# Kernel optimization log

Measured on AMD Instinct MI355X. Metric: run time of the kernel, lower is better.

## Reference

```python
import jax, jax.numpy as jnp
import numpy as np

D_K = 64

def setup_inputs() -> dict:
    key = jax.random.key(0)
    kq, kk, kv = jax.random.split(key, 3)
    B, Lq, Lk, d = 32, 2048, 2048, D_K
    return {
        "query": jax.random.normal(kq, (B, Lq, d), dtype=jnp.float32),
        "key": jax.random.normal(kk, (B, Lk, d), dtype=jnp.float32),
        "value": jax.random.normal(kv, (B, Lk, d), dtype=jnp.float32),
    }

def reference(query, key, value):
    d_k = query.shape[-1]
    scale = 1.0 / jnp.sqrt(jnp.asarray(d_k, query.dtype))
    scores = jnp.einsum('nqd,nkd->nqk', query, key) * scale  # (B, Lq, Lk)
    attn = jax.nn.softmax(scores, axis=-1)  # masked=None -> plain softmax; dropout p=0.0 is identity
    return jnp.einsum('nqk,nkd->nqd', attn, value)  # (B, Lq, d_v)
```

## Files before the change

### kernel.cpp

```cpp
#include <hip/hip_runtime.h>


#define NB   32
#define LSEQ 2048
#define DH   64
#define BM   64
#define BN   64
#define NIT  (LSEQ / BN)

typedef __attribute__((ext_vector_type(8)))  __bf16 bf16x8;
typedef __attribute__((ext_vector_type(16))) float  f32x16;

union BF8 { bf16x8 v; unsigned short u[8]; unsigned u32[4]; uint4 q; };

__device__ __forceinline__ unsigned short f2bf(float f) {
    unsigned int u = __builtin_bit_cast(unsigned int, f);
    u += 0x7fffu + ((u >> 16) & 1u);
    return (unsigned short)(u >> 16);
}

__device__ __forceinline__ unsigned pack_bf2(float a, float b) {
    unsigned ua = __builtin_bit_cast(unsigned, a) + 0x8000u;
    unsigned ub = __builtin_bit_cast(unsigned, b) + 0x8000u;
    return __builtin_amdgcn_perm(ub, ua, 0x07060302u);
}

__device__ __forceinline__ float fast_exp2(float x) {
#if __has_builtin(__builtin_amdgcn_exp2f)
    return __builtin_amdgcn_exp2f(x);
#else
    return exp2f(x);
#endif
}

__device__ __forceinline__ void load_lds16(const void* g, void* l) {
    __builtin_amdgcn_global_load_lds(
        (const __attribute__((address_space(1))) void*)g,
        (__attribute__((address_space(3))) void*)l, 16, 0, 0);
}

#define KBLK ((NB * LSEQ * DH) / (256 * 8))
__global__ __launch_bounds__(256)
void prep(const float* __restrict__ Kg, const float* __restrict__ Vg,
          unsigned short* __restrict__ Kb, unsigned short* __restrict__ Vt) {
    __shared__ unsigned short T[64 * 65];
    const int tid = threadIdx.x;
    if (blockIdx.x < KBLK) {
        const size_t idx = ((size_t)blockIdx.x * 256 + tid) * 8;
        float4 f0 = ((const float4*)(Kg + idx))[0];
        float4 f1 = ((const float4*)(Kg + idx))[1];
        BF8 t;
        t.u[0]=f2bf(f0.x); t.u[1]=f2bf(f0.y); t.u[2]=f2bf(f0.z); t.u[3]=f2bf(f0.w);
        t.u[4]=f2bf(f1.x); t.u[5]=f2bf(f1.y); t.u[6]=f2bf(f1.z); t.u[7]=f2bf(f1.w);
        *(bf16x8*)&Kb[idx] = t.v;
    } else {
        const int bx = blockIdx.x - KBLK;
        const int b  = bx >> 5;
        const int nt = bx & 31;
        const int nl = tid >> 2;
        const int dc = (tid & 3) * 16;
        const float* src = Vg + (((size_t)b * LSEQ + nt * 64 + nl) * DH + dc);
        float4 f0 = ((const float4*)src)[0];
        float4 f1 = ((const float4*)src)[1];
        float4 f2 = ((const float4*)src)[2];
        float4 f3 = ((const float4*)src)[3];
        float vv[16] = {f0.x,f0.y,f0.z,f0.w, f1.x,f1.y,f1.z,f1.w,
                        f2.x,f2.y,f2.z,f2.w, f3.x,f3.y,f3.z,f3.w};
        #pragma unroll
        for (int i = 0; i < 16; ++i)
            T[(dc + i) * 65 + nl] = f2bf(vv[i]);
        __syncthreads();
        #pragma unroll
        for (int i = 0; i < 2; ++i) {
            const int CH = i * 256 + tid;
            const int d  = CH >> 3;
            const int cc = CH & 7;
            const int nloc = (cc ^ (d & 7)) * 8;
            BF8 o;
            #pragma unroll
            for (int j = 0; j < 8; ++j) o.u[j] = T[d * 65 + nloc + j];
            *(bf16x8*)&Vt[(((size_t)(b * 64 + d)) * 256 + nt * 8 + cc) * 8] = o.v;
        }
    }
}

__global__ __launch_bounds__(256, 4)
void attn_fwd(const unsigned short* __restrict__ Kb,
              const unsigned short* __restrict__ Vt,
              const float* __restrict__ Qg,
              float* __restrict__ Og) {
    __shared__ __align__(16) unsigned short Vlds[2][BN * DH];
    __shared__ __align__(16) float Mrg[2][64][36];
    __shared__ float Lsh[2][32];

    const int tid  = threadIdx.x;
    const int wave = tid >> 6;
    const int lane = tid & 63;
    const int m32  = lane & 31;
    const int h    = lane >> 5;
    const int qh   = wave >> 1;
    const int kvh  = wave & 1;
    const int b    = blockIdx.y;
    const int qt   = blockIdx.x;

    const float qscale = 0.18033688011112042f;
    const int qrow = qt * BM + qh * 32 + m32;
    bf16x8 qf[4];
    {
        const float* qp = Qg + ((size_t)(b * LSEQ + qrow)) * DH;
        #pragma unroll
        for (int kt = 0; kt < 4; ++kt) {
            const float* p4 = qp + kt * 16 + h * 8;
            float4 f0 = ((const float4*)p4)[0];
            float4 f1 = ((const float4*)p4)[1];
            BF8 t;
            t.u[0]=f2bf(f0.x*qscale); t.u[1]=f2bf(f0.y*qscale);
            t.u[2]=f2bf(f0.z*qscale); t.u[3]=f2bf(f0.w*qscale);
            t.u[4]=f2bf(f1.x*qscale); t.u[5]=f2bf(f1.y*qscale);
            t.u[6]=f2bf(f1.z*qscale); t.u[7]=f2bf(f1.w*qscale);
            qf[kt] = t.v;
        }
    }

    const char* kptr = (const char*)Kb
        + ((size_t)b * LSEQ + (kvh * 32 + m32)) * (DH * 2) + h * 16;

    int vidx[2][2];
    #pragma unroll
    for (int dt = 0; dt < 2; ++dt)
        #pragma unroll
        for (int kt = 0; kt < 2; ++kt) {
            const int d  = dt * 32 + m32;
            const int cc = kvh * 4 + kt * 2 + h;
            vidx[dt][kt] = (d * 8 + (cc ^ (d & 7))) * 8;
        }

    const char* vgb = (const char*)Vt + (size_t)b * (DH * LSEQ * 2);
    const int CH0 = wave * 128 + lane;
    const int CH1 = CH0 + 64;
    const int voff0 = (CH0 >> 3) * (LSEQ * 2) + (CH0 & 7) * 16;
    const int voff1 = (CH1 >> 3) * (LSEQ * 2) + (CH1 & 7) * 16;
    load_lds16(vgb + voff0, (char*)&Vlds[0][0] + wave * 2048);
    load_lds16(vgb + voff1, (char*)&Vlds[0][0] + wave * 2048 + 1024);

    f32x16 o0, o1;
    #pragma unroll
    for (int i = 0; i < 16; ++i) { o0[i] = 0.f; o1[i] = 0.f; }
    float l_run = 0.f;

    for (int nt = 0; nt < NIT; ++nt) {
        const int cur = nt & 1;
        __syncthreads();

        BF8 kf[4];
        {
            const char* ka = kptr + nt * (BN * DH * 2);
            #pragma unroll
            for (int kt = 0; kt < 4; ++kt)
                kf[kt].q = *(const uint4*)(ka + kt * 32);
        }
        if (nt + 1 < NIT) {
            char* vl = (char*)&Vlds[cur ^ 1][0] + wave * 2048;
            load_lds16(vgb + (nt + 1) * 128 + voff0, vl);
            load_lds16(vgb + (nt + 1) * 128 + voff1, vl + 1024);
        }

        f32x16 s;
        #pragma unroll
        for (int i = 0; i < 16; ++i) s[i] = 0.f;
        #pragma unroll
        for (int kt = 0; kt < 4; ++kt)
            s = __builtin_amdgcn_mfma_f32_32x32x16_bf16(kf[kt].v, qf[kt], s, 0, 0, 0);

        BF8 vf[2][2];
        #pragma unroll
        for (int dt = 0; dt < 2; ++dt)
            #pragma unroll
            for (int kt = 0; kt < 2; ++kt)
                vf[dt][kt].v = *(const bf16x8*)&Vlds[cur][vidx[dt][kt]];

        float e[16];
        #pragma unroll
        for (int r = 0; r < 16; ++r) e[r] = fast_exp2(s[r]);
        #pragma unroll
        for (int g = 0; g < 4; ++g)
            l_run += ((e[4*g] + e[4*g+1]) + (e[4*g+2] + e[4*g+3]));
        unsigned pk[8];
        #pragma unroll
        for (int g = 0; g < 4; ++g) {
            pk[2*g]   = pack_bf2(e[4*g],   e[4*g+1]);
            pk[2*g+1] = pack_bf2(e[4*g+2], e[4*g+3]);
        }

        const unsigned sA0 = h ? pk[0] : pk[2];
        const unsigned sA1 = h ? pk[1] : pk[3];
        const unsigned sB0 = h ? pk[4] : pk[6];
        const unsigned sB1 = h ? pk[5] : pk[7];
        const unsigned rA0 = __shfl_xor((int)sA0, 32, 64);
        const unsigned rA1 = __shfl_xor((int)sA1, 32, 64);
        const unsigned rB0 = __shfl_xor((int)sB0, 32, 64);
        const unsigned rB1 = __shfl_xor((int)sB1, 32, 64);
        BF8 p0, p1;
        p0.u32[0] = h ? rA0 : pk[0];  p0.u32[1] = h ? rA1 : pk[1];
        p0.u32[2] = h ? pk[2] : rA0;  p0.u32[3] = h ? pk[3] : rA1;
        p1.u32[0] = h ? rB0 : pk[4];  p1.u32[1] = h ? rB1 : pk[5];
        p1.u32[2] = h ? pk[6] : rB0;  p1.u32[3] = h ? pk[7] : rB1;

        o0 = __builtin_amdgcn_mfma_f32_32x32x16_bf16(vf[0][0].v, p0.v, o0, 0, 0, 0);
        o0 = __builtin_amdgcn_mfma_f32_32x32x16_bf16(vf[0][1].v, p1.v, o0, 0, 0, 0);
        o1 = __builtin_amdgcn_mfma_f32_32x32x16_bf16(vf[1][0].v, p0.v, o1, 0, 0, 0);
        o1 = __builtin_amdgcn_mfma_f32_32x32x16_bf16(vf[1][1].v, p1.v, o1, 0, 0, 0);
    }

    const float l2 = l_run + __shfl_xor(l_run, 32, 64);
    if (kvh) {
        float* mp = &Mrg[qh][lane][0];
        #pragma unroll
        for (int g = 0; g < 4; ++g) {
            *(float4*)(mp + 4*g)      = (float4){o0[4*g], o0[4*g+1], o0[4*g+2], o0[4*g+3]};
            *(float4*)(mp + 16 + 4*g) = (float4){o1[4*g], o1[4*g+1], o1[4*g+2], o1[4*g+3]};
        }
        if (h == 0) Lsh[qh][m32] = l2;
    }
    __syncthreads();
    if (!kvh) {
        const float* mp = &Mrg[qh][lane][0];
        #pragma unroll
        for (int g = 0; g < 4; ++g) {
            float4 a = *(const float4*)(mp + 4*g);
            float4 c = *(const float4*)(mp + 16 + 4*g);
            o0[4*g] += a.x; o0[4*g+1] += a.y; o0[4*g+2] += a.z; o0[4*g+3] += a.w;
            o1[4*g] += c.x; o1[4*g+1] += c.y; o1[4*g+2] += c.z; o1[4*g+3] += c.w;
        }
        const float inv = 1.0f / (l2 + Lsh[qh][m32]);
        float* op = Og + ((size_t)(b * LSEQ + qrow)) * DH;
        #pragma unroll
        for (int t = 0; t < 2; ++t)
            #pragma unroll
            for (int g = 0; g < 4; ++g) {
                float4 v;
                v.x = (t ? o1[4*g+0] : o0[4*g+0]) * inv;
                v.y = (t ? o1[4*g+1] : o0[4*g+1]) * inv;
                v.z = (t ? o1[4*g+2] : o0[4*g+2]) * inv;
                v.w = (t ? o1[4*g+3] : o0[4*g+3]) * inv;
                *(float4*)(op + t * 32 + g * 8 + h * 4) = v;
            }
    }
}

extern "C" void kernel_launch(void* const* d_in, const int* in_sizes, int n_in,
                              void* d_out, int out_size, void* d_ws, size_t ws_size,
                              hipStream_t stream) {
    const float* Q = (const float*)d_in[0];
    const float* K = (const float*)d_in[1];
    const float* V = (const float*)d_in[2];
    float* O = (float*)d_out;

    unsigned short* Kb = (unsigned short*)d_ws;
    unsigned short* Vt = (unsigned short*)d_ws + 4u * 1024u * 1024u;

    prep<<<dim3(KBLK + NB * (LSEQ / 64)), dim3(256), 0, stream>>>(K, V, Kb, Vt);
    attn_fwd<<<dim3(LSEQ / BM, NB), dim3(256), 0, stream>>>(Kb, Vt, Q, O);
}
```

Before: 168.1 us.

## Stage K tiles through LDS with swizzled layout and async double-buffering

The prep kernel now writes bf16 K in an XOR-swizzled chunk order. The attention kernel loads each K tile into double-buffered LDS with global_load_lds, alongside V, instead of having each wave read K fragments directly from global memory inside the loop. This takes the global load latency for K off the critical path of the QK^T MFMAs and lets the block share one tile load. In exchange, LDS use grows to 32KB per block, the merge buffers are aliased onto the same memory (which needs an extra barrier), and occupancy with 4 blocks per CU may be affected.

```diff
diff --git a/kernel.cpp b/kernel.cpp
--- a/kernel.cpp
+++ b/kernel.cpp
@@ -39,20 +39,26 @@
         (__attribute__((address_space(3))) void*)l, 16, 0, 0);
 }
 
-#define KBLK ((NB * LSEQ * DH) / (256 * 8))
+#define KBLK ((NB * LSEQ * 8) / 256)
 __global__ __launch_bounds__(256)
 void prep(const float* __restrict__ Kg, const float* __restrict__ Vg,
           unsigned short* __restrict__ Kb, unsigned short* __restrict__ Vt) {
     __shared__ unsigned short T[64 * 65];
     const int tid = threadIdx.x;
     if (blockIdx.x < KBLK) {
-        const size_t idx = ((size_t)blockIdx.x * 256 + tid) * 8;
-        float4 f0 = ((const float4*)(Kg + idx))[0];
-        float4 f1 = ((const float4*)(Kg + idx))[1];
+        const int CH  = blockIdx.x * 256 + tid;
+        const int b   = CH >> 14;
+        const int rem = CH & 16383;
+        const int n   = rem >> 3;
+        const int cc  = rem & 7;
+        const int c   = cc ^ (n & 7);
+        const float* src = Kg + (((size_t)b * LSEQ + n) * DH + c * 8);
+        float4 f0 = ((const float4*)src)[0];
+        float4 f1 = ((const float4*)src)[1];
         BF8 t;
         t.u[0]=f2bf(f0.x); t.u[1]=f2bf(f0.y); t.u[2]=f2bf(f0.z); t.u[3]=f2bf(f0.w);
         t.u[4]=f2bf(f1.x); t.u[5]=f2bf(f1.y); t.u[6]=f2bf(f1.z); t.u[7]=f2bf(f1.w);
-        *(bf16x8*)&Kb[idx] = t.v;
+        *(bf16x8*)&Kb[(size_t)CH * 8] = t.v;
     } else {
         const int bx = blockIdx.x - KBLK;
         const int b  = bx >> 5;
@@ -89,9 +95,11 @@
               const unsigned short* __restrict__ Vt,
               const float* __restrict__ Qg,
               float* __restrict__ Og) {
-    __shared__ __align__(16) unsigned short Vlds[2][BN * DH];
-    __shared__ __align__(16) float Mrg[2][64][36];
-    __shared__ float Lsh[2][32];
+    __shared__ __align__(16) char smem[32768];
+    unsigned short* Kl = (unsigned short*)smem;
+    unsigned short* Vl = (unsigned short*)(smem + 16384);
+    float* Mrg = (float*)smem;
+    float* Lsh = (float*)(smem + 18432);
 
     const int tid  = threadIdx.x;
     const int wave = tid >> 6;
@@ -122,9 +130,13 @@
         }
     }
 
-    const char* kptr = (const char*)Kb
-        + ((size_t)b * LSEQ + (kvh * 32 + m32)) * (DH * 2) + h * 16;
-
+    int kidx[4];
+    #pragma unroll
+    for (int kt = 0; kt < 4; ++kt) {
+        const int n  = kvh * 32 + m32;
+        const int cc = kt * 2 + h;
+        kidx[kt] = (n * 8 + (cc ^ (n & 7))) * 8;
+    }
     int vidx[2][2];
     #pragma unroll
     for (int dt = 0; dt < 2; ++dt)
@@ -135,13 +147,21 @@
             vidx[dt][kt] = (d * 8 + (cc ^ (d & 7))) * 8;
         }
 
+    const char* kgb = (const char*)Kb + (size_t)b * (LSEQ * DH * 2);
     const char* vgb = (const char*)Vt + (size_t)b * (DH * LSEQ * 2);
     const int CH0 = wave * 128 + lane;
     const int CH1 = CH0 + 64;
     const int voff0 = (CH0 >> 3) * (LSEQ * 2) + (CH0 & 7) * 16;
     const int voff1 = (CH1 >> 3) * (LSEQ * 2) + (CH1 & 7) * 16;
-    load_lds16(vgb + voff0, (char*)&Vlds[0][0] + wave * 2048);
-    load_lds16(vgb + voff1, (char*)&Vlds[0][0] + wave * 2048 + 1024);
+
+    {
+        char* kd = smem + wave * 2048;
+        char* vd = smem + 16384 + wave * 2048;
+        load_lds16(kgb + CH0 * 16, kd);
+        load_lds16(kgb + CH1 * 16, kd + 1024);
+        load_lds16(vgb + voff0, vd);
+        load_lds16(vgb + voff1, vd + 1024);
+    }
 
     f32x16 o0, o1;
     #pragma unroll
@@ -152,32 +172,32 @@
         const int cur = nt & 1;
         __syncthreads();
 
-        BF8 kf[4];
-        {
-            const char* ka = kptr + nt * (BN * DH * 2);
-            #pragma unroll
-            for (int kt = 0; kt < 4; ++kt)
-                kf[kt].q = *(const uint4*)(ka + kt * 32);
-        }
         if (nt + 1 < NIT) {
-            char* vl = (char*)&Vlds[cur ^ 1][0] + wave * 2048;
-            load_lds16(vgb + (nt + 1) * 128 + voff0, vl);
-            load_lds16(vgb + (nt + 1) * 128 + voff1, vl + 1024);
-        }
-
+            char* kd = smem + (cur ^ 1) * 8192 + wave * 2048;
+            char* vd = smem + 16384 + (cur ^ 1) * 8192 + wave * 2048;
+            load_lds16(kgb + (nt + 1) * 8192 + CH0 * 16, kd);
+            load_lds16(kgb + (nt + 1) * 8192 + CH1 * 16, kd + 1024);
+            load_lds16(vgb + (nt + 1) * 128 + voff0, vd);
+            load_lds16(vgb + (nt + 1) * 128 + voff1, vd + 1024);
+        }
+
+        const unsigned short* kb = Kl + cur * 4096;
         f32x16 s;
         #pragma unroll
         for (int i = 0; i < 16; ++i) s[i] = 0.f;
         #pragma unroll
-        for (int kt = 0; kt < 4; ++kt)
-            s = __builtin_amdgcn_mfma_f32_32x32x16_bf16(kf[kt].v, qf[kt], s, 0, 0, 0);
-
+        for (int kt = 0; kt < 4; ++kt) {
+            bf16x8 kf = *(const bf16x8*)&kb[kidx[kt]];
+            s = __builtin_amdgcn_mfma_f32_32x32x16_bf16(kf, qf[kt], s, 0, 0, 0);
+        }
+
+        const unsigned short* vb = Vl + cur * 4096;
         BF8 vf[2][2];
         #pragma unroll
         for (int dt = 0; dt < 2; ++dt)
             #pragma unroll
             for (int kt = 0; kt < 2; ++kt)
-                vf[dt][kt].v = *(const bf16x8*)&Vlds[cur][vidx[dt][kt]];
+                vf[dt][kt].v = *(const bf16x8*)&vb[vidx[dt][kt]];
 
         float e[16];
         #pragma unroll
@@ -213,18 +233,19 @@
     }
 
     const float l2 = l_run + __shfl_xor(l_run, 32, 64);
+    __syncthreads();
     if (kvh) {
-        float* mp = &Mrg[qh][lane][0];
+        float* mp = Mrg + ((size_t)qh * 64 + lane) * 36;
         #pragma unroll
         for (int g = 0; g < 4; ++g) {
             *(float4*)(mp + 4*g)      = (float4){o0[4*g], o0[4*g+1], o0[4*g+2], o0[4*g+3]};
             *(float4*)(mp + 16 + 4*g) = (float4){o1[4*g], o1[4*g+1], o1[4*g+2], o1[4*g+3]};
         }
-        if (h == 0) Lsh[qh][m32] = l2;
+        if (h == 0) Lsh[qh * 32 + m32] = l2;
     }
     __syncthreads();
     if (!kvh) {
-        const float* mp = &Mrg[qh][lane][0];
+        const float* mp = Mrg + ((size_t)qh * 64 + lane) * 36;
         #pragma unroll
         for (int g = 0; g < 4; ++g) {
             float4 a = *(const float4*)(mp + 4*g);
@@ -232,7 +253,7 @@
             o0[4*g] += a.x; o0[4*g+1] += a.y; o0[4*g+2] += a.z; o0[4*g+3] += a.w;
             o1[4*g] += c.x; o1[4*g+1] += c.y; o1[4*g+2] += c.z; o1[4*g+3] += c.w;
         }
-        const float inv = 1.0f / (l2 + Lsh[qh][m32]);
+        const float inv = 1.0f / (l2 + Lsh[qh * 32 + m32]);
         float* op = Og + ((size_t)(b * LSEQ + qrow)) * DH;
         #pragma unroll
         for (int t = 0; t < 2; ++t)
```

Result: faster. 139.7 us (-16.9%).
